# Kernel optimization log

Measured on AMD Instinct MI355X. Metric: run time of the kernel, lower is better.

Reference implementation:

```python
import jax, jax.numpy as jnp
import numpy as np

B, CIN, H, W = 32, 256, 32, 32
DK, DV, HEADS, OUT = 128, 128, 8, 256
DKH = DK // HEADS
DVH = DV // HEADS


def _conv1x1(x, w, b):
    # x: [B,C,H,W], w: [O,C], b: [O]
    return jnp.einsum('bchw,oc->bohw', x, w) + b[None, :, None, None]


def setup_inputs() -> dict:
    key = jax.random.key(0)
    ks = jax.random.split(key, 7)
    s = 0.02
    return {
        'x': jax.random.normal(ks[0], (B, CIN, H, W), jnp.float32),
        'w_qkv': jax.random.normal(ks[1], (2 * DK + DV, CIN), jnp.float32) * s,
        'b_qkv': jnp.zeros((2 * DK + DV,), jnp.float32),
        'w_attn': jax.random.normal(ks[2], (DV, DV), jnp.float32) * s,
        'b_attn': jnp.zeros((DV,), jnp.float32),
        'w_out': jax.random.normal(ks[3], (OUT - DV, CIN), jnp.float32) * s,
        'b_out': jnp.zeros((OUT - DV,), jnp.float32),
    }


def reference(x, w_qkv, b_qkv, w_attn, b_attn, w_out, b_out):
    b = x.shape[0]
    N = H * W
    # parallel conv branch (kernel_size=1 so spatial dims match attention branch)
    conv_out = _conv1x1(x, w_out, b_out)  # [B, OUT-DV, H, W]
    # qkv projection
    qkv = _conv1x1(x, w_qkv, b_qkv)  # [B, 2*DK+DV, H, W]
    q, k, v = jnp.split(qkv, [DK, 2 * DK], axis=1)
    q = q.reshape(b, HEADS, DKH, N) * (DKH ** -0.5)
    k = k.reshape(b, HEADS, DKH, N)
    v = v.reshape(b, HEADS, DVH, N)
    # scaled dot-product attention over the N=H*W flattened positions
    logits = jnp.einsum('bhdq,bhdk->bhqk', q, k)  # [B,heads,N,N]
    weights = jax.nn.softmax(logits, axis=-1)
    attn = jnp.einsum('bhqk,bhdk->bhdq', weights, v)  # [B,heads,DVH,N]
    attn = attn.reshape(b, DV, H, W)
    attn = _conv1x1(attn, w_attn, b_attn)
    return jnp.concatenate([conv_out, attn], axis=1)
```

## Files before the change

### kernel.cpp

```cpp
#include <hip/hip_runtime.h>
#include <hip/hip_bf16.h>

#define BATCH 32
#define CIN   256
#define NPOS  1024
#define DKC   128
#define DVC   128
#define HEADS 8
#define OUTC  256

typedef __bf16 bf16x8 __attribute__((ext_vector_type(8)));
typedef __bf16 bf16x4 __attribute__((ext_vector_type(4)));
typedef float  f32x4  __attribute__((ext_vector_type(4)));
typedef float  f32x16 __attribute__((ext_vector_type(16)));
typedef unsigned u32x4 __attribute__((ext_vector_type(4)));

#define QSCALE 0.3606737602f

__device__ inline bf16x8 load8(const __bf16* p) {
    return *reinterpret_cast<const bf16x8*>(p);
}
__device__ inline f32x4 fzero4() {
    f32x4 z;
#pragma unroll
    for (int i = 0; i < 4; ++i) z[i] = 0.0f;
    return z;
}
__device__ inline float fexp2(float x) {
#if __has_builtin(__builtin_amdgcn_exp2f)
    return __builtin_amdgcn_exp2f(x);
#else
    return exp2f(x);
#endif
}

__global__ __launch_bounds__(256) void detect_dtype(const unsigned short* __restrict__ xraw,
                                                    int* __restrict__ flag) {
    __shared__ int s;
    if (threadIdx.x == 0) s = 0;
    __syncthreads();
    int cnt = 0;
#pragma unroll
    for (int j = 0; j < 64; ++j) {
        unsigned short u = xraw[threadIdx.x * 64 + j];
        unsigned int e = (u >> 7) & 0xFF;
        if (e >= 0x92) cnt++;
    }
    if (cnt) atomicAdd(&s, cnt);
    __syncthreads();
    if (threadIdx.x == 0) *flag = (s > 0) ? 1 : 0;
}

#define CV_WQKV 98304
#define CV_WOUT (CV_WQKV + 32768)
#define CV_BQKV (CV_WOUT + 384)
#define CV_BOUT (CV_BQKV + 128)
#define CV_WATT (CV_BOUT + 16384)
#define CV_BATT (CV_WATT + 128)
__global__ __launch_bounds__(256) void convert_all(
    const void* __restrict__ w_qkv, const void* __restrict__ b_qkv,
    const void* __restrict__ w_attn, const void* __restrict__ b_attn,
    const void* __restrict__ w_out, const void* __restrict__ b_out,
    __bf16* __restrict__ wcat, __bf16* __restrict__ bcat,
    __bf16* __restrict__ w_attnc, __bf16* __restrict__ b_attnc,
    const int* __restrict__ flag) {
    int i = blockIdx.x * 256 + threadIdx.x;
    const void* src; __bf16* dst; int j;
    if      (i < CV_WQKV) { src = w_qkv;  j = i;           dst = wcat + i; }
    else if (i < CV_WOUT) { src = w_out;  j = i - CV_WQKV; dst = wcat + i; }
    else if (i < CV_BQKV) { src = b_qkv;  j = i - CV_WOUT; dst = bcat + j; }
    else if (i < CV_BOUT) { src = b_out;  j = i - CV_BQKV; dst = bcat + 384 + j; }
    else if (i < CV_WATT) { src = w_attn; j = i - CV_BOUT; dst = w_attnc + j; }
    else if (i < CV_BATT) { src = b_attn; j = i - CV_WATT; dst = b_attnc + j; }
    else return;
    if (*flag) *dst = (__bf16)((const float*)src)[j];
    else       *dst = ((const __bf16*)src)[j];
}

__global__ __launch_bounds__(256) void xpose(
    const void* __restrict__ xv, __bf16* __restrict__ xT,
    const int* __restrict__ flag) {
    __shared__ __bf16 tile[64][72];
    bool isf32 = (*flag != 0);
    int b = blockIdx.z, c0 = blockIdx.y * 64, n0 = blockIdx.x * 64;
    int t = threadIdx.x, nl = t & 63, cb = t >> 6;
#pragma unroll
    for (int cs = 0; cs < 16; ++cs) {
        int cw = cs * 4 + cb;
        size_t gi = ((size_t)b * CIN + c0 + cw) * NPOS + n0 + nl;
        float v = isf32 ? ((const float*)xv)[gi] : (float)((const __bf16*)xv)[gi];
        tile[nl][cw] = (__bf16)v;
    }
    __syncthreads();
    int row = t >> 2, seg = t & 3;
    bf16x8 v0 = *reinterpret_cast<const bf16x8*>(&tile[row][seg * 16]);
    bf16x8 v1 = *reinterpret_cast<const bf16x8*>(&tile[row][seg * 16 + 8]);
    __bf16* dst = xT + ((size_t)b * NPOS + n0 + row) * CIN + c0 + seg * 16;
    *reinterpret_cast<bf16x8*>(dst)     = v0;
    *reinterpret_cast<bf16x8*>(dst + 8) = v1;
}

__global__ __launch_bounds__(512, 4) void qkv_conv_gemm2(
    const __bf16* __restrict__ xT,
    const __bf16* __restrict__ wcat,
    const __bf16* __restrict__ bcat,
    __bf16* __restrict__ q_ws,
    __bf16* __restrict__ k_ws,
    __bf16* __restrict__ v_ws,
    void* __restrict__ out,
    const int* __restrict__ flag)
{
    int b   = blockIdx.y;
    int n0  = blockIdx.x * 64;
    int wave = threadIdx.x >> 6;
    int lane = threadIdx.x & 63;
    int quad = lane >> 4, colid = lane & 15;
    int row0 = (wave >> 2) * 256 + (wave & 3) * 64;

    const __bf16* xp = xT + ((size_t)b * NPOS + n0) * CIN;
    const __bf16* wp = wcat + (size_t)(row0 + colid) * CIN + quad * 8;
    const __bf16* bp = xp + (size_t)colid * CIN + quad * 8;

    f32x4 acc[4][4];
#pragma unroll
    for (int rt = 0; rt < 4; ++rt)
#pragma unroll
        for (int st = 0; st < 4; ++st) acc[rt][st] = fzero4();

#pragma unroll
    for (int k0 = 0; k0 < CIN; k0 += 32) {
        bf16x8 aA[4], bB[4];
#pragma unroll
        for (int rt = 0; rt < 4; ++rt)
            aA[rt] = load8(wp + (size_t)rt * 16 * CIN + k0);
#pragma unroll
        for (int st = 0; st < 4; ++st)
            bB[st] = load8(bp + (size_t)st * 16 * CIN + k0);
#pragma unroll
        for (int rt = 0; rt < 4; ++rt)
#pragma unroll
            for (int st = 0; st < 4; ++st)
                acc[rt][st] = __builtin_amdgcn_mfma_f32_16x16x32_bf16(aA[rt], bB[st], acc[rt][st], 0, 0, 0);
    }

    bool isf32 = (*flag != 0);
#pragma unroll
    for (int rt = 0; rt < 4; ++rt) {
        int obase = row0 + rt * 16;
        float bias[4];
#pragma unroll
        for (int r = 0; r < 4; ++r) bias[r] = (float)bcat[obase + quad * 4 + r];

        if (obase < DKC) {
            int h = obase >> 4;
            __bf16* qb = q_ws + (((size_t)b * HEADS + h) * NPOS + n0) * 16 + quad * 4;
#pragma unroll
            for (int st = 0; st < 4; ++st) {
                bf16x4 ov;
#pragma unroll
                for (int r = 0; r < 4; ++r)
                    ov[r] = (__bf16)((acc[rt][st][r] + bias[r]) * QSCALE);
                *reinterpret_cast<bf16x4*>(qb + (size_t)(st * 16 + colid) * 16) = ov;
            }
        } else if (obase < 2 * DKC) {
            int h = (obase - DKC) >> 4;
            __bf16* kb = k_ws + (((size_t)b * HEADS + h) * NPOS + n0) * 16 + quad * 4;
#pragma unroll
            for (int st = 0; st < 4; ++st) {
                bf16x4 ov;
#pragma unroll
                for (int r = 0; r < 4; ++r)
                    ov[r] = (__bf16)(acc[rt][st][r] + bias[r]);
                *reinterpret_cast<bf16x4*>(kb + (size_t)(st * 16 + colid) * 16) = ov;
            }
        } else if (obase < 384) {
            int h = (obase - 2 * DKC) >> 4;
            __bf16* vb = v_ws + (((size_t)b * HEADS + h) * 16 + quad * 4) * NPOS + n0 + colid;
#pragma unroll
            for (int r = 0; r < 4; ++r)
#pragma unroll
                for (int st = 0; st < 4; ++st)
                    vb[(size_t)r * NPOS + st * 16] = (__bf16)(acc[rt][st][r] + bias[r]);
        } else {
            int oc = obase - 384 + quad * 4;
#pragma unroll
            for (int r = 0; r < 4; ++r) {
                size_t ob = ((size_t)b * OUTC + oc + r) * NPOS + n0 + colid;
#pragma unroll
                for (int st = 0; st < 4; ++st) {
                    float v = acc[rt][st][r] + bias[r];
                    if (isf32) ((float*)out)[ob + st * 16] = v;
                    else       ((__bf16*)out)[ob + st * 16] = (__bf16)v;
                }
            }
        }
    }
}

#define OSTR 136
__global__ __launch_bounds__(512, 4) void attention_kernel(
    const __bf16* __restrict__ q_ws,
    const __bf16* __restrict__ k_ws,
    const __bf16* __restrict__ v_ws,
    const __bf16* __restrict__ w_attn,
    const __bf16* __restrict__ b_attn,
    void* __restrict__ out,
    const int* __restrict__ flag)
{
    __shared__ __align__(16) __bf16 olds[64][OSTR];
    int b    = blockIdx.x;
    int nq0  = blockIdx.y * 64;
    int wave = threadIdx.x >> 6;
    int lane = threadIdx.x & 63;
    int l5   = lane & 31, hi = lane >> 5;
    int h    = wave;
    int bh   = b * HEADS + h;

    const __bf16* qp = q_ws + (size_t)bh * NPOS * 16;
    const __bf16* kp = k_ws + (size_t)bh * NPOS * 16;
    const __bf16* vp = v_ws + (size_t)bh * 16 * NPOS;

    bf16x8 qB0 = load8(qp + (size_t)(nq0 + l5) * 16 + hi * 8);
    bf16x8 qB1 = load8(qp + (size_t)(nq0 + 32 + l5) * 16 + hi * 8);

    bf16x8 vA0, vA1;
#pragma unroll
    for (int i = 0; i < 8; ++i) { vA0[i] = (__bf16)1.0f; vA1[i] = (__bf16)1.0f; }
    const __bf16* vrow = vp + (size_t)l5 * NPOS + hi * 8;

    f32x16 zero16;
#pragma unroll
    for (int i = 0; i < 16; ++i) zero16[i] = 0.0f;
    f32x16 acc0 = zero16, acc1 = zero16;

#pragma unroll 2
    for (int nk0 = 0; nk0 < NPOS; nk0 += 32) {
        bf16x8 kA = load8(kp + (size_t)(nk0 + l5) * 16 + hi * 8);
        if (l5 < 16) {
            vA0 = load8(vrow + nk0);
            vA1 = load8(vrow + nk0 + 16);
        }
#pragma unroll
        for (int half = 0; half < 2; ++half) {
            f32x16 st = __builtin_amdgcn_mfma_f32_32x32x16_bf16(
                kA, half ? qB1 : qB0, zero16, 0, 0, 0);
            unsigned w[8];
#pragma unroll
            for (int m = 0; m < 4; ++m) {
                float e0 = fexp2(st[4 * m + 0]);
                float e1 = fexp2(st[4 * m + 1]);
                float e2 = fexp2(st[4 * m + 2]);
                float e3 = fexp2(st[4 * m + 3]);
                unsigned lo, hw;
                asm("v_cvt_pk_bf16_f32 %0, %1, %2" : "=v"(lo) : "v"(e0), "v"(e1));
                asm("v_cvt_pk_bf16_f32 %0, %1, %2" : "=v"(hw) : "v"(e2), "v"(e3));
                w[2 * m]     = lo;
                w[2 * m + 1] = hw;
            }
            asm("v_permlane32_swap_b32 %0, %1" : "+v"(w[0]), "+v"(w[2]));
            asm("v_permlane32_swap_b32 %0, %1" : "+v"(w[1]), "+v"(w[3]));
            asm("v_permlane32_swap_b32 %0, %1" : "+v"(w[4]), "+v"(w[6]));
            asm("v_permlane32_swap_b32 %0, %1" : "+v"(w[5]), "+v"(w[7]));
            u32x4 t1 = {w[0], w[1], w[2], w[3]};
            u32x4 t2 = {w[4], w[5], w[6], w[7]};
            bf16x8 pB1 = __builtin_bit_cast(bf16x8, t1);
            bf16x8 pB2 = __builtin_bit_cast(bf16x8, t2);
            if (half) {
                acc1 = __builtin_amdgcn_mfma_f32_32x32x16_bf16(vA0, pB1, acc1, 0, 0, 0);
                acc1 = __builtin_amdgcn_mfma_f32_32x32x16_bf16(vA1, pB2, acc1, 0, 0, 0);
            } else {
                acc0 = __builtin_amdgcn_mfma_f32_32x32x16_bf16(vA0, pB1, acc0, 0, 0, 0);
                acc0 = __builtin_amdgcn_mfma_f32_32x32x16_bf16(vA1, pB2, acc0, 0, 0, 0);
            }
        }
    }
#pragma unroll
    for (int half = 0; half < 2; ++half) {
        const f32x16& acc = half ? acc1 : acc0;
        float inv = 1.0f / acc[8];
        bf16x4 o0, o1;
#pragma unroll
        for (int r = 0; r < 4; ++r) {
            o0[r] = (__bf16)(acc[r] * inv);
            o1[r] = (__bf16)(acc[4 + r] * inv);
        }
        __bf16* ol = &olds[32 * half + l5][h * 16 + 4 * hi];
        *reinterpret_cast<bf16x4*>(ol)     = o0;
        *reinterpret_cast<bf16x4*>(ol + 8) = o1;
    }
    __syncthreads();

    int quad = lane >> 4, colid = lane & 15;
    int row0 = h * 16;
    f32x4 pacc[4];
#pragma unroll
    for (int st = 0; st < 4; ++st) pacc[st] = fzero4();
#pragma unroll
    for (int k0 = 0; k0 < DVC; k0 += 32) {
        bf16x8 a = load8(w_attn + (size_t)(row0 + colid) * DVC + k0 + quad * 8);
#pragma unroll
        for (int st = 0; st < 4; ++st) {
            bf16x8 bb = *reinterpret_cast<const bf16x8*>(&olds[st * 16 + colid][k0 + quad * 8]);
            pacc[st] = __builtin_amdgcn_mfma_f32_16x16x32_bf16(a, bb, pacc[st], 0, 0, 0);
        }
    }
    bool isf32 = (*flag != 0);
#pragma unroll
    for (int r = 0; r < 4; ++r) {
        int o = row0 + quad * 4 + r;
        float bias = (float)b_attn[o];
#pragma unroll
        for (int st = 0; st < 4; ++st) {
            int n = nq0 + st * 16 + colid;
            float v = pacc[st][r] + bias;
            size_t oi = ((size_t)b * OUTC + DVC + o) * NPOS + n;
            if (isf32) ((float*)out)[oi] = v;
            else       ((__bf16*)out)[oi] = (__bf16)v;
        }
    }
}

extern "C" void kernel_launch(void* const* d_in, const int* in_sizes, int n_in,
                              void* d_out, int out_size, void* d_ws, size_t ws_size,
                              hipStream_t stream) {
    const void* x      = d_in[0];
    const void* w_qkv  = d_in[1];
    const void* b_qkv  = d_in[2];
    const void* w_attn = d_in[3];
    const void* b_attn = d_in[4];
    const void* w_out  = d_in[5];
    const void* b_out  = d_in[6];

    char* ws = (char*)d_ws;
    int*    flag    = (int*)ws;
    __bf16* wcat    = (__bf16*)(ws + (1u << 20));
    __bf16* bcat    = (__bf16*)(ws + (3u << 19));
    __bf16* w_attnc = (__bf16*)(ws + (7u << 18));
    __bf16* b_attnc = (__bf16*)(ws + (1u << 21));
    __bf16* xT      = (__bf16*)(ws + (1u << 22));
    __bf16* q_ws    = (__bf16*)(ws + (28u << 20));
    __bf16* k_ws    = (__bf16*)(ws + (36u << 20));
    __bf16* v_ws    = (__bf16*)(ws + (44u << 20));

    detect_dtype<<<1, 256, 0, stream>>>((const unsigned short*)x, flag);
    convert_all<<<(CV_BATT + 255) / 256, 256, 0, stream>>>(
        w_qkv, b_qkv, w_attn, b_attn, w_out, b_out,
        wcat, bcat, w_attnc, b_attnc, flag);
    xpose<<<dim3(NPOS / 64, CIN / 64, BATCH), 256, 0, stream>>>(x, xT, flag);

    qkv_conv_gemm2<<<dim3(NPOS / 64, BATCH), 512, 0, stream>>>(
        xT, wcat, bcat, q_ws, k_ws, v_ws, d_out, flag);
    attention_kernel<<<dim3(BATCH, NPOS / 64), 512, 0, stream>>>(
        q_ws, k_ws, v_ws, w_attnc, b_attnc, d_out, flag);
}
```

Baseline: 177.5 us.

## Fuse input transpose into QKV GEMM via LDS and prefetch K/V in attention

After: 164.7 us. -7.2%, faster.

```diff
diff --git a/kernel.cpp b/kernel.cpp
--- a/kernel.cpp
+++ b/kernel.cpp
@@ -77,31 +77,8 @@
     else       *dst = ((const __bf16*)src)[j];
 }
 
-__global__ __launch_bounds__(256) void xpose(
-    const void* __restrict__ xv, __bf16* __restrict__ xT,
-    const int* __restrict__ flag) {
-    __shared__ __bf16 tile[64][72];
-    bool isf32 = (*flag != 0);
-    int b = blockIdx.z, c0 = blockIdx.y * 64, n0 = blockIdx.x * 64;
-    int t = threadIdx.x, nl = t & 63, cb = t >> 6;
-#pragma unroll
-    for (int cs = 0; cs < 16; ++cs) {
-        int cw = cs * 4 + cb;
-        size_t gi = ((size_t)b * CIN + c0 + cw) * NPOS + n0 + nl;
-        float v = isf32 ? ((const float*)xv)[gi] : (float)((const __bf16*)xv)[gi];
-        tile[nl][cw] = (__bf16)v;
-    }
-    __syncthreads();
-    int row = t >> 2, seg = t & 3;
-    bf16x8 v0 = *reinterpret_cast<const bf16x8*>(&tile[row][seg * 16]);
-    bf16x8 v1 = *reinterpret_cast<const bf16x8*>(&tile[row][seg * 16 + 8]);
-    __bf16* dst = xT + ((size_t)b * NPOS + n0 + row) * CIN + c0 + seg * 16;
-    *reinterpret_cast<bf16x8*>(dst)     = v0;
-    *reinterpret_cast<bf16x8*>(dst + 8) = v1;
-}
-
-__global__ __launch_bounds__(512, 4) void qkv_conv_gemm2(
-    const __bf16* __restrict__ xT,
+__global__ __launch_bounds__(512, 4) void qkv_conv_gemm3(
+    const void* __restrict__ xv,
     const __bf16* __restrict__ wcat,
     const __bf16* __restrict__ bcat,
     __bf16* __restrict__ q_ws,
@@ -110,16 +87,28 @@
     void* __restrict__ out,
     const int* __restrict__ flag)
 {
+    __shared__ __bf16 xs[64][264];
+    bool isf32 = (*flag != 0);
     int b   = blockIdx.y;
     int n0  = blockIdx.x * 64;
-    int wave = threadIdx.x >> 6;
-    int lane = threadIdx.x & 63;
+    int t   = threadIdx.x;
+    int nl  = t & 63, cb = t >> 6;
+
+#pragma unroll
+    for (int cs = 0; cs < 32; ++cs) {
+        int c = cs * 8 + cb;
+        size_t gi = ((size_t)b * CIN + c) * NPOS + n0 + nl;
+        float v = isf32 ? ((const float*)xv)[gi] : (float)((const __bf16*)xv)[gi];
+        xs[nl][c] = (__bf16)v;
+    }
+    __syncthreads();
+
+    int wave = t >> 6;
+    int lane = t & 63;
     int quad = lane >> 4, colid = lane & 15;
     int row0 = (wave >> 2) * 256 + (wave & 3) * 64;
 
-    const __bf16* xp = xT + ((size_t)b * NPOS + n0) * CIN;
     const __bf16* wp = wcat + (size_t)(row0 + colid) * CIN + quad * 8;
-    const __bf16* bp = xp + (size_t)colid * CIN + quad * 8;
 
     f32x4 acc[4][4];
 #pragma unroll
@@ -135,7 +124,7 @@
             aA[rt] = load8(wp + (size_t)rt * 16 * CIN + k0);
 #pragma unroll
         for (int st = 0; st < 4; ++st)
-            bB[st] = load8(bp + (size_t)st * 16 * CIN + k0);
+            bB[st] = *reinterpret_cast<const bf16x8*>(&xs[st * 16 + colid][k0 + quad * 8]);
 #pragma unroll
         for (int rt = 0; rt < 4; ++rt)
 #pragma unroll
@@ -143,7 +132,6 @@
                 acc[rt][st] = __builtin_amdgcn_mfma_f32_16x16x32_bf16(aA[rt], bB[st], acc[rt][st], 0, 0, 0);
     }
 
-    bool isf32 = (*flag != 0);
 #pragma unroll
     for (int rt = 0; rt < 4; ++rt) {
         int obase = row0 + rt * 16;
@@ -233,12 +221,20 @@
     for (int i = 0; i < 16; ++i) zero16[i] = 0.0f;
     f32x16 acc0 = zero16, acc1 = zero16;
 
+    bf16x8 kA = load8(kp + (size_t)l5 * 16 + hi * 8);
+    if (l5 < 16) {
+        vA0 = load8(vrow);
+        vA1 = load8(vrow + 16);
+    }
+
 #pragma unroll 2
     for (int nk0 = 0; nk0 < NPOS; nk0 += 32) {
-        bf16x8 kA = load8(kp + (size_t)(nk0 + l5) * 16 + hi * 8);
+        int nkn = (nk0 + 32) & (NPOS - 1);
+        bf16x8 kA_n = load8(kp + (size_t)(nkn + l5) * 16 + hi * 8);
+        bf16x8 vA0_n = vA0, vA1_n = vA1;
         if (l5 < 16) {
-            vA0 = load8(vrow + nk0);
-            vA1 = load8(vrow + nk0 + 16);
+            vA0_n = load8(vrow + nkn);
+            vA1_n = load8(vrow + nkn + 16);
         }
 #pragma unroll
         for (int half = 0; half < 2; ++half) {
@@ -273,6 +269,7 @@
                 acc0 = __builtin_amdgcn_mfma_f32_32x32x16_bf16(vA1, pB2, acc0, 0, 0, 0);
             }
         }
+        kA = kA_n; vA0 = vA0_n; vA1 = vA1_n;
     }
 #pragma unroll
     for (int half = 0; half < 2; ++half) {
@@ -337,7 +334,6 @@
     __bf16* bcat    = (__bf16*)(ws + (3u << 19));
     __bf16* w_attnc = (__bf16*)(ws + (7u << 18));
     __bf16* b_attnc = (__bf16*)(ws + (1u << 21));
-    __bf16* xT      = (__bf16*)(ws + (1u << 22));
     __bf16* q_ws    = (__bf16*)(ws + (28u << 20));
     __bf16* k_ws    = (__bf16*)(ws + (36u << 20));
     __bf16* v_ws    = (__bf16*)(ws + (44u << 20));
@@ -346,10 +342,9 @@
     convert_all<<<(CV_BATT + 255) / 256, 256, 0, stream>>>(
         w_qkv, b_qkv, w_attn, b_attn, w_out, b_out,
         wcat, bcat, w_attnc, b_attnc, flag);
-    xpose<<<dim3(NPOS / 64, CIN / 64, BATCH), 256, 0, stream>>>(x, xT, flag);
-
-    qkv_conv_gemm2<<<dim3(NPOS / 64, BATCH), 512, 0, stream>>>(
-        xT, wcat, bcat, q_ws, k_ws, v_ws, d_out, flag);
+
+    qkv_conv_gemm3<<<dim3(NPOS / 64, BATCH), 512, 0, stream>>>(
+        x, wcat, bcat, q_ws, k_ws, v_ws, d_out, flag);
     attention_kernel<<<dim3(BATCH, NPOS / 64), 512, 0, stream>>>(
         q_ws, k_ws, v_ws, w_attnc, b_attnc, d_out, flag);
 }
```
